# Performance work log

Measured on AMD Instinct MI355X. Metric: run time of the kernel, lower is better.

Reference implementation:

```python
import jax, jax.numpy as jnp
import numpy as np


def setup_inputs() -> dict:
    key = jax.random.key(0)
    k1, k2, k3, k4 = jax.random.split(key, 4)
    B, H, N, D = 4, 16, 2048, 128
    return {
        "q": jax.random.normal(k1, (B, H, N, D), dtype=jnp.float32),
        "k": jax.random.normal(k2, (B, H, N, D), dtype=jnp.float32),
        "v": jax.random.normal(k3, (B, H, N, D), dtype=jnp.float32),
        "g": jax.random.normal(k4, (B, H, N, 1), dtype=jnp.float32),
    }


def reference(q, k, v, g):
    """GLA recurrence: S_t = l_t * S_{t-1} + (1 - l_t) * k_t v_t^T; o_t = q_t S_t."""
    scale = 1.0
    B, H, N, D = q.shape
    lambd = jax.nn.sigmoid(g)                      # [B,H,N,1]
    qs = q * scale
    # time-major for scan: [N,B,H,...]
    qt = jnp.moveaxis(qs, 2, 0)
    kt = jnp.moveaxis(k, 2, 0)
    vt = jnp.moveaxis(v, 2, 0)
    lt = jnp.moveaxis(lambd, 2, 0)[..., None]      # [N,B,H,1,1]
    S0 = jnp.zeros((B, H, D, D), dtype=q.dtype)

    def step(S, inp):
        q_t, k_t, v_t, l_t = inp
        kv = jnp.einsum('bhd,bhe->bhde', k_t, v_t)  # rank-1 update per head
        S = l_t * S + (1.0 - l_t) * kv
        o = jnp.einsum('bhd,bhde->bhe', q_t, S)
        return S, o

    _, outs = jax.lax.scan(step, S0, (qt, kt, vt, lt))  # outs: [N,B,H,D]
    return jnp.moveaxis(outs, 0, 2)                     # [B,H,N,D]
```

## Files before the change

kernel.cpp:

```cpp
#include <hip/hip_runtime.h>

#define NTOK 2048
#define DD   128
#define CHK  64
#define PCH  16
#define EW   32

typedef __attribute__((ext_vector_type(8))) short bf16x8;
typedef __attribute__((ext_vector_type(4))) float f32x4;
typedef unsigned short u16;

#define MFMA(a,b,c) __builtin_amdgcn_mfma_f32_16x16x32_bf16(a,b,c,0,0,0)

__device__ __forceinline__ u16 f2bf(float f){
  union { float f; unsigned u; } x; x.f = f;
  return (u16)((x.u + 0x7fffu + ((x.u >> 16) & 1u)) >> 16);
}
__device__ __forceinline__ int swz(int r, int c, int re){
  int b = (r*re + c)*2;
  return b ^ ((r & 7) << 4);
}
__device__ __forceinline__ void lds_w1(u16* a, int r, int c, int re, u16 v){
  *(u16*)((char*)a + swz(r,c,re)) = v;
}
__device__ __forceinline__ void lds_w4(u16* a, int r, int c, int re, ushort4 v){
  *(ushort4*)((char*)a + swz(r,c,re)) = v;
}
__device__ __forceinline__ bf16x8 lds_r8(const u16* a, int r, int c, int re){
  return *(const bf16x8*)((const char*)a + swz(r,c,re));
}

__global__ __launch_bounds__(256) void gla_part(
    const float* __restrict__ Qg, const float* __restrict__ Kg,
    const float* __restrict__ Vg, const float* __restrict__ Gg,
    float* __restrict__ Og, float* __restrict__ Smid, float* __restrict__ Bpre)
{
  __shared__ u16 sKh [CHK*DD];
  __shared__ u16 sKhT[DD*CHK];
  __shared__ u16 sVT [EW*CHK];
  __shared__ u16 sST [EW*DD];
  __shared__ u16 sPb [CHK*CHK];

  const int tid = threadIdx.x;
  const int w = tid >> 6, l = tid & 63, lr = l & 15, lh = l >> 4;
  const int gid  = blockIdx.x;
  const int head = (gid & 7) | (((gid >> 6) & 7) << 3);
  const int e0   = ((gid >> 3) & 3) * EW;
  const int part = (gid >> 5) & 1;
  const int tbase = part * (PCH*CHK);

  const float* Qh = Qg + (size_t)head*NTOK*DD;
  const float* Kh = Kg + (size_t)head*NTOK*DD;
  const float* Vh = Vg + (size_t)head*NTOK*DD;
  const float* Gh = Gg + (size_t)head*NTOK;
  float* Oh = Og + (size_t)head*NTOK*DD;

  f32x4 S00 = {}, S01 = {}, S10 = {}, S11 = {};
  float4 kpre[8], vpre[2], qpre[8];
  float gst;

  auto loads = [&](int c){
    const int t0 = tbase + c*CHK;
    gst = Gh[t0 + l];
    const int srow = t0 + (tid >> 2);
    const float* kp = Kh + (size_t)srow*DD + 4*(tid & 3);
    #pragma unroll
    for (int i=0;i<8;++i) kpre[i] = *(const float4*)(kp + 16*i);
    const float* vp = Vh + (size_t)srow*DD + e0 + 4*(tid & 3);
    #pragma unroll
    for (int i=0;i<2;++i) vpre[i] = *(const float4*)(vp + 16*i);
    const float* qp = Qh + (size_t)(t0 + w*16 + lr)*DD + lh*8;
    #pragma unroll
    for (int i=0;i<4;++i){
      qpre[2*i]   = *(const float4*)(qp + 32*i);
      qpre[2*i+1] = *(const float4*)(qp + 32*i + 4);
    }
  };

  float ckl_s, cq, scc, bl63;
  auto scan = [&](){
    float li = 1.f/(1.f + expf(-gst));
    float x  = log2f(li);
    #pragma unroll
    for (int off=1; off<64; off<<=1){
      float y = __shfl_up(x, off, 64);
      if (l >= off) x += y;
    }
    bl63 = __shfl(x, 63, 64);
    scc  = exp2f(bl63);
    cq   = exp2f(__shfl(x, w*16 + lr, 64));
    float cklr = exp2f(-x) * (1.f - li);
    ckl_s = __shfl(cklr, w*16 + (l >> 2), 64);
  };

  loads(0);
  scan();
  float bsum = 0.f;
  if (part == 1 && e0 == 0 && tid == 0) Bpre[head*PCH] = 0.f;

  for (int c=0; c<PCH; ++c){
    __syncthreads();

    const int srow = tid >> 2;
    #pragma unroll
    for (int i=0;i<8;++i){
      float4 kf = kpre[i];
      int d = 4*((tid & 3) + 4*i);
      u16 b0=f2bf(kf.x*ckl_s), b1=f2bf(kf.y*ckl_s), b2=f2bf(kf.z*ckl_s), b3=f2bf(kf.w*ckl_s);
      lds_w4(sKh, srow, d, DD, make_ushort4(b0,b1,b2,b3));
      lds_w1(sKhT, d+0, srow, CHK, b0);
      lds_w1(sKhT, d+1, srow, CHK, b1);
      lds_w1(sKhT, d+2, srow, CHK, b2);
      lds_w1(sKhT, d+3, srow, CHK, b3);
    }
    #pragma unroll
    for (int i=0;i<2;++i){
      float4 vf = vpre[i];
      int e = 4*((tid & 3) + 4*i);
      lds_w1(sVT, e+0, srow, CHK, f2bf(vf.x));
      lds_w1(sVT, e+1, srow, CHK, f2bf(vf.y));
      lds_w1(sVT, e+2, srow, CHK, f2bf(vf.z));
      lds_w1(sVT, e+3, srow, CHK, f2bf(vf.w));
    }
    {
      const int dbase = w*32 + lh*4;
      #pragma unroll
      for (int r=0;r<4;++r){
        lds_w1(sST, lr,    dbase + r,      DD, f2bf(S00[r]));
        lds_w1(sST, 16+lr, dbase + r,      DD, f2bf(S01[r]));
        lds_w1(sST, lr,    dbase + 16 + r, DD, f2bf(S10[r]));
        lds_w1(sST, 16+lr, dbase + 16 + r, DD, f2bf(S11[r]));
      }
    }
    bf16x8 qA[4];
    #pragma unroll
    for (int ks=0;ks<4;++ks){
      float4 a = qpre[2*ks], b = qpre[2*ks+1];
      bf16x8 t;
      t[0]=(short)f2bf(a.x*cq); t[1]=(short)f2bf(a.y*cq);
      t[2]=(short)f2bf(a.z*cq); t[3]=(short)f2bf(a.w*cq);
      t[4]=(short)f2bf(b.x*cq); t[5]=(short)f2bf(b.y*cq);
      t[6]=(short)f2bf(b.z*cq); t[7]=(short)f2bf(b.w*cq);
      qA[ks] = t;
    }
    if (c+1 < PCH) loads(c+1);
    __syncthreads();

    f32x4 oacc0 = {}, oacc1 = {};
    f32x4 p0 = {}, p1 = {}, p2 = {}, p3 = {};
    #pragma unroll
    for (int ks=0;ks<4;++ks){
      const int kk = ks*32 + lh*8;
      bf16x8 a = qA[ks];
      oacc0 = MFMA(a, lds_r8(sST, lr,    kk, DD), oacc0);
      oacc1 = MFMA(a, lds_r8(sST, 16+lr, kk, DD), oacc1);
      p0 = MFMA(a, lds_r8(sKh, lr,    kk, DD), p0);
      p1 = MFMA(a, lds_r8(sKh, 16+lr, kk, DD), p1);
      p2 = MFMA(a, lds_r8(sKh, 32+lr, kk, DD), p2);
      p3 = MFMA(a, lds_r8(sKh, 48+lr, kk, DD), p3);
    }
    {
      const int t = w*16 + lh*4;
      #pragma unroll
      for (int r=0;r<4;++r){
        int tt = t + r;
        lds_w1(sPb, tt, lr,    CHK, f2bf((lr    <= tt) ? p0[r] : 0.f));
        lds_w1(sPb, tt, 16+lr, CHK, f2bf((16+lr <= tt) ? p1[r] : 0.f));
        lds_w1(sPb, tt, 32+lr, CHK, f2bf((32+lr <= tt) ? p2[r] : 0.f));
        lds_w1(sPb, tt, 48+lr, CHK, f2bf((48+lr <= tt) ? p3[r] : 0.f));
      }
    }
    asm volatile("s_waitcnt lgkmcnt(0)" ::: "memory");
    __builtin_amdgcn_sched_barrier(0);

    #pragma unroll
    for (int k2=0;k2<2;++k2){
      const int kk = k2*32 + lh*8;
      bf16x8 vb0 = lds_r8(sVT, lr,    kk, CHK);
      bf16x8 vb1 = lds_r8(sVT, 16+lr, kk, CHK);
      bf16x8 pa  = lds_r8(sPb, w*16 + lr, kk, CHK);
      oacc0 = MFMA(pa, vb0, oacc0);
      oacc1 = MFMA(pa, vb1, oacc1);
      bf16x8 ka0 = lds_r8(sKhT, w*32 + lr,      kk, CHK);
      bf16x8 ka1 = lds_r8(sKhT, w*32 + 16 + lr, kk, CHK);
      S00 = MFMA(ka0, vb0, S00);
      S01 = MFMA(ka0, vb1, S01);
      S10 = MFMA(ka1, vb0, S10);
      S11 = MFMA(ka1, vb1, S11);
    }
    #pragma unroll
    for (int r=0;r<4;++r){ S00[r]*=scc; S01[r]*=scc; S10[r]*=scc; S11[r]*=scc; }

    {
      float* op = Oh + (size_t)(tbase + c*CHK + w*16 + lh*4)*DD + e0;
      #pragma unroll
      for (int r=0;r<4;++r){
        op[r*DD + lr]      = oacc0[r];
        op[r*DD + 16 + lr] = oacc1[r];
      }
    }
    if (c+1 < PCH){
      if (part == 1){
        bsum += bl63;
        if (e0 == 0 && tid == 0) Bpre[head*PCH + c + 1] = bsum;
      }
      scan();
    }
  }

  if (part == 0){
    float* sm = Smid + (size_t)head*DD*DD + e0;
    const int dbase = w*32 + lh*4;
    #pragma unroll
    for (int r=0;r<4;++r){
      sm[(size_t)(dbase + r)*DD + lr]           = S00[r];
      sm[(size_t)(dbase + r)*DD + 16 + lr]      = S01[r];
      sm[(size_t)(dbase + 16 + r)*DD + lr]      = S10[r];
      sm[(size_t)(dbase + 16 + r)*DD + 16 + lr] = S11[r];
    }
  }
}

__global__ __launch_bounds__(256) void gla_fix(
    const float* __restrict__ Qg, const float* __restrict__ Gg,
    float* __restrict__ Og, const float* __restrict__ Smid,
    const float* __restrict__ Bpre)
{
  __shared__ u16 sS[DD*DD];
  const int tid = threadIdx.x;
  const int w = tid >> 6, l = tid & 63, lr = l & 15, lh = l >> 4;
  const int head = blockIdx.x >> 4, c = blockIdx.x & 15;
  const int t0 = PCH*CHK + c*CHK;

  {
    const int d = tid >> 1, eb = (tid & 1)*64;
    const float* sp = Smid + (size_t)head*DD*DD + (size_t)d*DD + eb;
    #pragma unroll
    for (int j=0;j<16;++j){
      float4 f = *(const float4*)(sp + 4*j);
      lds_w1(sS, eb + 4*j + 0, d, DD, f2bf(f.x));
      lds_w1(sS, eb + 4*j + 1, d, DD, f2bf(f.y));
      lds_w1(sS, eb + 4*j + 2, d, DD, f2bf(f.z));
      lds_w1(sS, eb + 4*j + 3, d, DD, f2bf(f.w));
    }
  }
  float gst = Gg[(size_t)head*NTOK + t0 + l];
  float li = 1.f/(1.f + expf(-gst));
  float x  = log2f(li);
  #pragma unroll
  for (int off=1; off<64; off<<=1){
    float y = __shfl_up(x, off, 64);
    if (l >= off) x += y;
  }
  const float cq = exp2f(__shfl(x, w*16 + lr, 64) + Bpre[head*PCH + c]);

  bf16x8 qA[4];
  const float* qp = Qg + (size_t)head*NTOK*DD + (size_t)(t0 + w*16 + lr)*DD + lh*8;
  #pragma unroll
  for (int ks=0;ks<4;++ks){
    float4 a = *(const float4*)(qp + ks*32);
    float4 b = *(const float4*)(qp + ks*32 + 4);
    bf16x8 t;
    t[0]=(short)f2bf(a.x*cq); t[1]=(short)f2bf(a.y*cq);
    t[2]=(short)f2bf(a.z*cq); t[3]=(short)f2bf(a.w*cq);
    t[4]=(short)f2bf(b.x*cq); t[5]=(short)f2bf(b.y*cq);
    t[6]=(short)f2bf(b.z*cq); t[7]=(short)f2bf(b.w*cq);
    qA[ks] = t;
  }
  __syncthreads();

  f32x4 o0={},o1={},o2={},o3={},o4={},o5={},o6={},o7={};
  #pragma unroll
  for (int ks=0;ks<4;++ks){
    const int kk = ks*32 + lh*8;
    bf16x8 a = qA[ks];
    o0 = MFMA(a, lds_r8(sS, lr,      kk, DD), o0);
    o1 = MFMA(a, lds_r8(sS, 16+lr,   kk, DD), o1);
    o2 = MFMA(a, lds_r8(sS, 32+lr,   kk, DD), o2);
    o3 = MFMA(a, lds_r8(sS, 48+lr,   kk, DD), o3);
    o4 = MFMA(a, lds_r8(sS, 64+lr,   kk, DD), o4);
    o5 = MFMA(a, lds_r8(sS, 80+lr,   kk, DD), o5);
    o6 = MFMA(a, lds_r8(sS, 96+lr,   kk, DD), o6);
    o7 = MFMA(a, lds_r8(sS, 112+lr,  kk, DD), o7);
  }
  float* op = Og + (size_t)head*NTOK*DD + (size_t)(t0 + w*16 + lh*4)*DD;
  #pragma unroll
  for (int r=0;r<4;++r){
    op[r*DD + lr]       += o0[r];
    op[r*DD + 16 + lr]  += o1[r];
    op[r*DD + 32 + lr]  += o2[r];
    op[r*DD + 48 + lr]  += o3[r];
    op[r*DD + 64 + lr]  += o4[r];
    op[r*DD + 80 + lr]  += o5[r];
    op[r*DD + 96 + lr]  += o6[r];
    op[r*DD + 112 + lr] += o7[r];
  }
}

extern "C" void kernel_launch(void* const* d_in, const int* in_sizes, int n_in,
                              void* d_out, int out_size, void* d_ws, size_t ws_size,
                              hipStream_t stream)
{
  const float* q = (const float*)d_in[0];
  const float* k = (const float*)d_in[1];
  const float* v = (const float*)d_in[2];
  const float* g = (const float*)d_in[3];
  float* out = (float*)d_out;
  float* Smid = (float*)d_ws;
  float* Bpre = (float*)((char*)d_ws + (size_t)64*DD*DD*4);

  gla_part<<<dim3(512),  dim3(256), 0, stream>>>(q, k, v, g, out, Smid, Bpre);
  gla_fix <<<dim3(1024), dim3(256), 0, stream>>>(q, g, out, Smid, Bpre);
}
```

Baseline: 140.8 us.

## Remap K staging to 4x4 tiles for vectorized transposed LDS writes and custom barriers

After: 140.6 us. Within noise of the previous version (-0.2%).

```diff
diff --git a/kernel.cpp b/kernel.cpp
--- a/kernel.cpp
+++ b/kernel.cpp
@@ -11,6 +11,13 @@
 typedef unsigned short u16;
 
 #define MFMA(a,b,c) __builtin_amdgcn_mfma_f32_16x16x32_bf16(a,b,c,0,0,0)
+
+#define SBAR() do{ __builtin_amdgcn_sched_barrier(0); \
+  asm volatile("s_waitcnt lgkmcnt(0)" ::: "memory"); \
+  __builtin_amdgcn_s_barrier(); \
+  __builtin_amdgcn_sched_barrier(0); }while(0)
+#define VWAIT() do{ asm volatile("s_waitcnt vmcnt(0)" ::: "memory"); \
+  __builtin_amdgcn_sched_barrier(0); }while(0)
 
 __device__ __forceinline__ u16 f2bf(float f){
   union { float f; unsigned u; } x; x.f = f;
@@ -56,17 +63,23 @@
   float* Oh = Og + (size_t)head*NTOK*DD;
 
   f32x4 S00 = {}, S01 = {}, S10 = {}, S11 = {};
-  float4 kpre[8], vpre[2], qpre[8];
+  float4 kt[2][4];
+  float4 vpre[2], qpre[8];
   float gst;
+
+  const int q4 = (tid >> 4) * 4;
+  const int j0 = tid & 15;
 
   auto loads = [&](int c){
     const int t0 = tbase + c*CHK;
     gst = Gh[t0 + l];
-    const int srow = t0 + (tid >> 2);
-    const float* kp = Kh + (size_t)srow*DD + 4*(tid & 3);
-    #pragma unroll
-    for (int i=0;i<8;++i) kpre[i] = *(const float4*)(kp + 16*i);
-    const float* vp = Vh + (size_t)srow*DD + e0 + 4*(tid & 3);
+    #pragma unroll
+    for (int t=0;t<2;++t){
+      const float* kp = Kh + (size_t)(t0 + q4)*DD + (j0 + 16*t)*4;
+      #pragma unroll
+      for (int r=0;r<4;++r) kt[t][r] = *(const float4*)(kp + r*DD);
+    }
+    const float* vp = Vh + (size_t)(t0 + (tid>>2))*DD + e0 + 4*(tid&3);
     #pragma unroll
     for (int i=0;i<2;++i) vpre[i] = *(const float4*)(vp + 16*i);
     const float* qp = Qh + (size_t)(t0 + w*16 + lr)*DD + lh*8;
@@ -77,7 +90,7 @@
     }
   };
 
-  float ckl_s, cq, scc, bl63;
+  float cklr, cq, scc, bl63;
   auto scan = [&](){
     float li = 1.f/(1.f + expf(-gst));
     float x  = log2f(li);
@@ -89,8 +102,7 @@
     bl63 = __shfl(x, 63, 64);
     scc  = exp2f(bl63);
     cq   = exp2f(__shfl(x, w*16 + lr, 64));
-    float cklr = exp2f(-x) * (1.f - li);
-    ckl_s = __shfl(cklr, w*16 + (l >> 2), 64);
+    cklr = exp2f(-x) * (1.f - li);
   };
 
   loads(0);
@@ -99,38 +111,49 @@
   if (part == 1 && e0 == 0 && tid == 0) Bpre[head*PCH] = 0.f;
 
   for (int c=0; c<PCH; ++c){
-    __syncthreads();
-
-    const int srow = tid >> 2;
-    #pragma unroll
-    for (int i=0;i<8;++i){
-      float4 kf = kpre[i];
-      int d = 4*((tid & 3) + 4*i);
-      u16 b0=f2bf(kf.x*ckl_s), b1=f2bf(kf.y*ckl_s), b2=f2bf(kf.z*ckl_s), b3=f2bf(kf.w*ckl_s);
-      lds_w4(sKh, srow, d, DD, make_ushort4(b0,b1,b2,b3));
-      lds_w1(sKhT, d+0, srow, CHK, b0);
-      lds_w1(sKhT, d+1, srow, CHK, b1);
-      lds_w1(sKhT, d+2, srow, CHK, b2);
-      lds_w1(sKhT, d+3, srow, CHK, b3);
-    }
-    #pragma unroll
-    for (int i=0;i<2;++i){
-      float4 vf = vpre[i];
-      int e = 4*((tid & 3) + 4*i);
-      lds_w1(sVT, e+0, srow, CHK, f2bf(vf.x));
-      lds_w1(sVT, e+1, srow, CHK, f2bf(vf.y));
-      lds_w1(sVT, e+2, srow, CHK, f2bf(vf.z));
-      lds_w1(sVT, e+3, srow, CHK, f2bf(vf.w));
+    SBAR();
+    VWAIT();
+
+    {
+      const float cs0 = __shfl(cklr, q4+0, 64);
+      const float cs1 = __shfl(cklr, q4+1, 64);
+      const float cs2 = __shfl(cklr, q4+2, 64);
+      const float cs3 = __shfl(cklr, q4+3, 64);
+      #pragma unroll
+      for (int t=0;t<2;++t){
+        const int d0 = (j0 + 16*t)*4;
+        ushort4 r0 = make_ushort4(f2bf(kt[t][0].x*cs0), f2bf(kt[t][0].y*cs0), f2bf(kt[t][0].z*cs0), f2bf(kt[t][0].w*cs0));
+        ushort4 r1 = make_ushort4(f2bf(kt[t][1].x*cs1), f2bf(kt[t][1].y*cs1), f2bf(kt[t][1].z*cs1), f2bf(kt[t][1].w*cs1));
+        ushort4 r2 = make_ushort4(f2bf(kt[t][2].x*cs2), f2bf(kt[t][2].y*cs2), f2bf(kt[t][2].z*cs2), f2bf(kt[t][2].w*cs2));
+        ushort4 r3 = make_ushort4(f2bf(kt[t][3].x*cs3), f2bf(kt[t][3].y*cs3), f2bf(kt[t][3].z*cs3), f2bf(kt[t][3].w*cs3));
+        lds_w4(sKh, q4+0, d0, DD, r0);
+        lds_w4(sKh, q4+1, d0, DD, r1);
+        lds_w4(sKh, q4+2, d0, DD, r2);
+        lds_w4(sKh, q4+3, d0, DD, r3);
+        lds_w4(sKhT, d0+0, q4, CHK, make_ushort4(r0.x, r1.x, r2.x, r3.x));
+        lds_w4(sKhT, d0+1, q4, CHK, make_ushort4(r0.y, r1.y, r2.y, r3.y));
+        lds_w4(sKhT, d0+2, q4, CHK, make_ushort4(r0.z, r1.z, r2.z, r3.z));
+        lds_w4(sKhT, d0+3, q4, CHK, make_ushort4(r0.w, r1.w, r2.w, r3.w));
+      }
+    }
+    {
+      const int srow = tid >> 2;
+      #pragma unroll
+      for (int i=0;i<2;++i){
+        float4 vf = vpre[i];
+        int e = 4*((tid & 3) + 4*i);
+        lds_w1(sVT, e+0, srow, CHK, f2bf(vf.x));
+        lds_w1(sVT, e+1, srow, CHK, f2bf(vf.y));
+        lds_w1(sVT, e+2, srow, CHK, f2bf(vf.z));
+        lds_w1(sVT, e+3, srow, CHK, f2bf(vf.w));
+      }
     }
     {
       const int dbase = w*32 + lh*4;
-      #pragma unroll
-      for (int r=0;r<4;++r){
-        lds_w1(sST, lr,    dbase + r,      DD, f2bf(S00[r]));
-        lds_w1(sST, 16+lr, dbase + r,      DD, f2bf(S01[r]));
-        lds_w1(sST, lr,    dbase + 16 + r, DD, f2bf(S10[r]));
-        lds_w1(sST, 16+lr, dbase + 16 + r, DD, f2bf(S11[r]));
-      }
+      lds_w4(sST, lr,    dbase,      DD, make_ushort4(f2bf(S00[0]), f2bf(S00[1]), f2bf(S00[2]), f2bf(S00[3])));
+      lds_w4(sST, 16+lr, dbase,      DD, make_ushort4(f2bf(S01[0]), f2bf(S01[1]), f2bf(S01[2]), f2bf(S01[3])));
+      lds_w4(sST, lr,    dbase + 16, DD, make_ushort4(f2bf(S10[0]), f2bf(S10[1]), f2bf(S10[2]), f2bf(S10[3])));
+      lds_w4(sST, 16+lr, dbase + 16, DD, make_ushort4(f2bf(S11[0]), f2bf(S11[1]), f2bf(S11[2]), f2bf(S11[3])));
     }
     bf16x8 qA[4];
     #pragma unroll
@@ -144,7 +167,7 @@
       qA[ks] = t;
     }
     if (c+1 < PCH) loads(c+1);
-    __syncthreads();
+    SBAR();
 
     f32x4 oacc0 = {}, oacc1 = {};
     f32x4 p0 = {}, p1 = {}, p2 = {}, p3 = {};
```
